# Performance work log

Hardware: AMD Instinct MI355X
Metric: run time of the kernel (lower is better)

The kernel has to match this reference:

```python
import jax, jax.numpy as jnp
import numpy as np

SR = 44100.0
J, Q = 12, 16
W0 = 2.0 * np.pi      # MorletWavelet.freq_to_w_at_s(1.0, s=1.0) -> w = 2*pi*f*s
N_SIG = 3.0           # wavelet support = +/- N_SIG standard deviations


def _make_wavelet_bank():
    """Morlet filter bank: J octaves, Q steps/octave, highest freq = nyquist.
    Returns centered, zero-padded real/imag filter stacks of shape (K, Lmax)."""
    dt = 1.0 / SR
    nyq = SR / 2.0
    wavelets = []
    for j in range(J):
        for q in range(Q):
            f = nyq / (2.0 ** (j + q / Q))
            s = 1.0 / f                      # center freq f = W0/(2*pi*s) = 1/s
            M = int(np.ceil(N_SIG * s * SR))  # half support in samples
            t = np.arange(-M, M + 1) * dt
            psi = (np.pi ** -0.25) / np.sqrt(s) \
                * np.exp(1j * W0 * t / s) * np.exp(-0.5 * (t / s) ** 2)
            psi = psi / np.sum(np.abs(psi))   # L1 normalization
            wavelets.append(psi.astype(np.complex64))
    Lmax = max(len(p) for p in wavelets)       # odd (2*M_max + 1)
    bank = np.zeros((len(wavelets), Lmax), np.complex64)
    for i, p in enumerate(wavelets):
        left = (Lmax - len(p)) // 2            # center-pad each wavelet
        bank[i, left:left + len(p)] = p
    return bank


def setup_inputs() -> dict:
    key = jax.random.key(0)
    x = jax.random.normal(key, (2, 1, 32768), dtype=jnp.float32)
    bank = _make_wavelet_bank()
    return {
        "x": x,
        "filt_real": jnp.asarray(bank.real, dtype=jnp.float32),
        "filt_imag": jnp.asarray(bank.imag, dtype=jnp.float32),
    }


def _scat1d(x, filt_real, filt_imag):
    # x: (B, 1, T); filters: (K, L) with L odd. Equivalent to the torch path:
    # pad input by L//2, cross-correlate (F.conv1d) with each complex wavelet,
    # take the modulus. Done via FFT (same math, efficient for ~47k-tap kernels).
    K, L = filt_real.shape
    B, C, T = x.shape  # C == 1 (squeeze_channels=True)
    P = L // 2
    xp = jnp.pad(x[:, 0, :], ((0, 0), (P, P)))       # (B, T + 2P)
    n_full = xp.shape[-1] + L - 1
    N = 1 << (n_full - 1).bit_length()               # next pow2 FFT size
    X = jnp.fft.rfft(xp, N)                          # (B, N//2+1)
    Gr = jnp.fft.rfft(filt_real[:, ::-1], N)         # flip -> corr via conv
    Gi = jnp.fft.rfft(filt_imag[:, ::-1], N)         # (K, N//2+1)
    lo = L - 1                                       # valid-corr offset
    yr = jnp.fft.irfft(X[:, None, :] * Gr[None], N)[..., lo:lo + T]
    yi = jnp.fft.irfft(X[:, None, :] * Gi[None], N)[..., lo:lo + T]
    return jnp.sqrt(yr * yr + yi * yi)               # (B, K, T) modulus


def reference(x, filt_real, filt_imag):
    return _scat1d(x, filt_real, filt_imag)
```

## Files before the change

### kernel.cpp

```cpp
#include <hip/hip_runtime.h>
#include <math.h>

#define T_LEN   32768
#define NK      192
#define NB      2
#define KDIR    48
#define MAXM    56
#define BBLK    9216
#define WBLK    3872
#define GRIDX   (BBLK + WBLK)

struct SParams {
  int m1e[144];
  int voff[144];
  int slot[144];
  int ab[9];
};

__device__ __forceinline__ int j2_of_q(int q) {
  return 4 + (q >= 5) + (q >= 10) + (q >= 15);
}

__global__ __launch_bounds__(256) void k_vtab(float* __restrict__ ws, SParams P) {
  int ki = blockIdx.y;
  int slotc = P.slot[ki];
  int M1e = P.m1e[ki];
  float* dst = ws + P.voff[ki];
  int nent = 2 * M1e + 2;
  int k = ki + 48;
  int j = k >> 4, q = k & 15;
  float sig = 2.f * exp2f((float)(16 * j + q) * 0.0625f);
  float s1 = sig * 0.86602540378f;
  float gc = -0.5f / (s1 * s1);
  float om = 6.28318530718f / sig;
  float norm = 1.f / (2.50662827463f * s1 * erff((float)M1e / (1.41421356237f * s1)));
  #pragma unroll
  for (int e0 = 0; e0 < 4; ++e0) {
    int e = blockIdx.x * 1024 + e0 * 256 + threadIdx.x;
    if (e >= slotc) continue;
    if (e >= nent) { dst[2 * e] = 0.f; dst[2 * e + 1] = 0.f; continue; }
    float mm = (float)(e - M1e);
    float g = __expf(gc * mm * mm) * norm;
    float sn, cs; __sincosf(om * mm, &sn, &cs);
    dst[2 * e] = g * cs;
    dst[2 * e + 1] = g * sn;
  }
}

__global__ __launch_bounds__(256) void k_s1(const float* __restrict__ x,
                                            float* __restrict__ ws, SParams P) {
  __shared__ float red[16];
  const float* xb0 = x;
  const float* xb1 = x + T_LEN;
  int bx = blockIdx.x;
  int tid = threadIdx.x;

  if (bx < BBLK) {
    int j, base;
    if (bx < 512)       { j = 11; base = 0; }
    else if (bx < 1280) { j = 10; base = 512; }
    else if (bx < 2560) { j = 9;  base = 1280; }
    else if (bx < 4864) { j = 8;  base = 2560; }
    else                { j = 7;  base = 4864; }
    int rem = bx - base;
    int q = rem & 15, nidx = rem >> 4;
    int ki = 16 * (j - 3) + q;
    int d = 1 << j, J2 = j2_of_q(q);
    int M1e = P.m1e[ki];
    const float* vt = ws + P.voff[ki];
    int nd = (nidx - J2) * d;
    int ustart = nd - M1e;
    int it0 = (-ustart) >> 9; if (it0 < 0) it0 = 0;
    int itend = ((T_LEN - 1 - ustart) >> 9) + 1;
    int niter = P.slot[ki] >> 9; if (niter > itend) niter = itend;
    float ar0 = 0.f, ai0 = 0.f, ar1 = 0.f, ai1 = 0.f;
    int it = it0;
    for (; it + 4 <= niter; it += 4) {
      int mt0 = 2 * tid + (it << 9);
      float4 v0 = *(const float4*)(vt + 2 * mt0);
      float4 v1 = *(const float4*)(vt + 2 * (mt0 + 512));
      float4 v2 = *(const float4*)(vt + 2 * (mt0 + 1024));
      float4 v3 = *(const float4*)(vt + 2 * (mt0 + 1536));
      int u0 = ustart + mt0, u1 = u0 + 512, u2 = u0 + 1024, u3 = u0 + 1536;
      int c0 = min(max(u0, 0), T_LEN - 2), c1 = min(max(u1, 0), T_LEN - 2);
      int c2 = min(max(u2, 0), T_LEN - 2), c3 = min(max(u3, 0), T_LEN - 2);
      float2 a0 = *(const float2*)(xb0 + c0);
      float2 a1 = *(const float2*)(xb0 + c1);
      float2 a2 = *(const float2*)(xb0 + c2);
      float2 a3 = *(const float2*)(xb0 + c3);
      float2 b0 = *(const float2*)(xb1 + c0);
      float2 b1 = *(const float2*)(xb1 + c1);
      float2 b2 = *(const float2*)(xb1 + c2);
      float2 b3 = *(const float2*)(xb1 + c3);
      bool k0 = (unsigned)u0 <= (unsigned)(T_LEN - 2);
      bool k1 = (unsigned)u1 <= (unsigned)(T_LEN - 2);
      bool k2 = (unsigned)u2 <= (unsigned)(T_LEN - 2);
      bool k3 = (unsigned)u3 <= (unsigned)(T_LEN - 2);
      float xa00 = k0 ? a0.x : 0.f, xa01 = k0 ? a0.y : 0.f;
      float xa10 = k1 ? a1.x : 0.f, xa11 = k1 ? a1.y : 0.f;
      float xa20 = k2 ? a2.x : 0.f, xa21 = k2 ? a2.y : 0.f;
      float xa30 = k3 ? a3.x : 0.f, xa31 = k3 ? a3.y : 0.f;
      float xb00 = k0 ? b0.x : 0.f, xb01 = k0 ? b0.y : 0.f;
      float xb10 = k1 ? b1.x : 0.f, xb11 = k1 ? b1.y : 0.f;
      float xb20 = k2 ? b2.x : 0.f, xb21 = k2 ? b2.y : 0.f;
      float xb30 = k3 ? b3.x : 0.f, xb31 = k3 ? b3.y : 0.f;
      ar0 += v0.x * xa00; ai0 += v0.y * xa00; ar0 += v0.z * xa01; ai0 += v0.w * xa01;
      ar1 += v0.x * xb00; ai1 += v0.y * xb00; ar1 += v0.z * xb01; ai1 += v0.w * xb01;
      ar0 += v1.x * xa10; ai0 += v1.y * xa10; ar0 += v1.z * xa11; ai0 += v1.w * xa11;
      ar1 += v1.x * xb10; ai1 += v1.y * xb10; ar1 += v1.z * xb11; ai1 += v1.w * xb11;
      ar0 += v2.x * xa20; ai0 += v2.y * xa20; ar0 += v2.z * xa21; ai0 += v2.w * xa21;
      ar1 += v2.x * xb20; ai1 += v2.y * xb20; ar1 += v2.z * xb21; ai1 += v2.w * xb21;
      ar0 += v3.x * xa30; ai0 += v3.y * xa30; ar0 += v3.z * xa31; ai0 += v3.w * xa31;
      ar1 += v3.x * xb30; ai1 += v3.y * xb30; ar1 += v3.z * xb31; ai1 += v3.w * xb31;
    }
    for (; it < niter; ++it) {
      int mt = 2 * tid + (it << 9);
      float4 v = *(const float4*)(vt + 2 * mt);
      int u = ustart + mt;
      int uc = min(max(u, 0), T_LEN - 2);
      float2 pa = *(const float2*)(xb0 + uc);
      float2 pb = *(const float2*)(xb1 + uc);
      bool ok = (unsigned)u <= (unsigned)(T_LEN - 2);
      float x0 = ok ? pa.x : 0.f, x1 = ok ? pa.y : 0.f;
      float y0 = ok ? pb.x : 0.f, y1 = ok ? pb.y : 0.f;
      ar0 += v.x * x0; ai0 += v.y * x0; ar0 += v.z * x1; ai0 += v.w * x1;
      ar1 += v.x * y0; ai1 += v.y * y0; ar1 += v.z * y1; ai1 += v.w * y1;
    }
#define RED4(s_) ar0 += __shfl_xor(ar0, s_, 64); ai0 += __shfl_xor(ai0, s_, 64); \
                 ar1 += __shfl_xor(ar1, s_, 64); ai1 += __shfl_xor(ai1, s_, 64);
    RED4(1) RED4(2) RED4(4) RED4(8) RED4(16) RED4(32)
#undef RED4
    int wv = tid >> 6;
    if ((tid & 63) == 0) {
      red[4 * wv] = ar0; red[4 * wv + 1] = ai0;
      red[4 * wv + 2] = ar1; red[4 * wv + 3] = ai1;
    }
    __syncthreads();
    if (tid == 0) {
      ar0 = red[0] + red[4] + red[8] + red[12];
      ai0 = red[1] + red[5] + red[9] + red[13];
      ar1 = red[2] + red[6] + red[10] + red[14];
      ai1 = red[3] + red[7] + red[11] + red[15];
      float rev = (float)nd * exp2f(-(float)(16 * (j + 1) + q) * 0.0625f);
      rev -= floorf(rev);
      float sn, cs; __sincosf(rev * 6.28318530718f, &sn, &cs);
      int Ncu = (32767 >> j) + 17;
      float* ap = ws + P.ab[j - 3] + (q * 2) * Ncu * 2;
      *(float2*)(ap + 2 * nidx) = make_float2(ar0 * cs - ai0 * sn, ar0 * sn + ai0 * cs);
      *(float2*)(ap + 2 * (Ncu + nidx)) = make_float2(ar1 * cs - ai1 * sn, ar1 * sn + ai1 * cs);
    }
  } else {
    int wv = tid >> 6, lane = tid & 63;
    int wid = (bx - BBLK) * 4 + wv;
    int j, base;
    if (wid < 1056)      { j = 6; base = 0; }
    else if (wid < 3136) { j = 5; base = 1056; }
    else if (wid < 7264) { j = 4; base = 3136; }
    else                 { j = 3; base = 7264; }
    int rem = wid - base;
    int q = rem & 15, tile = rem >> 4;
    int ki = 16 * (j - 3) + q;
    int d = 1 << j, J2 = j2_of_q(q);
    int M1e = P.m1e[ki];
    const float* vt = ws + P.voff[ki];
    int r = lane >> 3, p = lane & 7;
    int nidx = tile * 8 + r;
    int nd = (nidx - J2) * d;
    int ustart = nd - M1e;
    int it0 = (-ustart) >> 4; if (it0 < 0) it0 = 0;
    int itend = ((T_LEN - 1 - ustart) >> 4) + 1;
    int niter = P.slot[ki] >> 4; if (niter > itend) niter = itend;
    float ar0 = 0.f, ai0 = 0.f, ar1 = 0.f, ai1 = 0.f;
    int it = it0;
    int pb2 = 2 * p;
    for (; it + 4 <= niter; it += 4) {
      int mt0 = pb2 + (it << 4);
      float4 v0 = *(const float4*)(vt + 2 * mt0);
      float4 v1 = *(const float4*)(vt + 2 * (mt0 + 16));
      float4 v2 = *(const float4*)(vt + 2 * (mt0 + 32));
      float4 v3 = *(const float4*)(vt + 2 * (mt0 + 48));
      int u0 = ustart + mt0, u1 = u0 + 16, u2 = u0 + 32, u3 = u0 + 48;
      int c0 = min(max(u0, 0), T_LEN - 2), c1 = min(max(u1, 0), T_LEN - 2);
      int c2 = min(max(u2, 0), T_LEN - 2), c3 = min(max(u3, 0), T_LEN - 2);
      float2 a0 = *(const float2*)(xb0 + c0);
      float2 a1 = *(const float2*)(xb0 + c1);
      float2 a2 = *(const float2*)(xb0 + c2);
      float2 a3 = *(const float2*)(xb0 + c3);
      float2 b0 = *(const float2*)(xb1 + c0);
      float2 b1 = *(const float2*)(xb1 + c1);
      float2 b2 = *(const float2*)(xb1 + c2);
      float2 b3 = *(const float2*)(xb1 + c3);
      bool k0 = (unsigned)u0 <= (unsigned)(T_LEN - 2);
      bool k1 = (unsigned)u1 <= (unsigned)(T_LEN - 2);
      bool k2 = (unsigned)u2 <= (unsigned)(T_LEN - 2);
      bool k3 = (unsigned)u3 <= (unsigned)(T_LEN - 2);
      float xa00 = k0 ? a0.x : 0.f, xa01 = k0 ? a0.y : 0.f;
      float xa10 = k1 ? a1.x : 0.f, xa11 = k1 ? a1.y : 0.f;
      float xa20 = k2 ? a2.x : 0.f, xa21 = k2 ? a2.y : 0.f;
      float xa30 = k3 ? a3.x : 0.f, xa31 = k3 ? a3.y : 0.f;
      float xb00 = k0 ? b0.x : 0.f, xb01 = k0 ? b0.y : 0.f;
      float xb10 = k1 ? b1.x : 0.f, xb11 = k1 ? b1.y : 0.f;
      float xb20 = k2 ? b2.x : 0.f, xb21 = k2 ? b2.y : 0.f;
      float xb30 = k3 ? b3.x : 0.f, xb31 = k3 ? b3.y : 0.f;
      ar0 += v0.x * xa00; ai0 += v0.y * xa00; ar0 += v0.z * xa01; ai0 += v0.w * xa01;
      ar1 += v0.x * xb00; ai1 += v0.y * xb00; ar1 += v0.z * xb01; ai1 += v0.w * xb01;
      ar0 += v1.x * xa10; ai0 += v1.y * xa10; ar0 += v1.z * xa11; ai0 += v1.w * xa11;
      ar1 += v1.x * xb10; ai1 += v1.y * xb10; ar1 += v1.z * xb11; ai1 += v1.w * xb11;
      ar0 += v2.x * xa20; ai0 += v2.y * xa20; ar0 += v2.z * xa21; ai0 += v2.w * xa21;
      ar1 += v2.x * xb20; ai1 += v2.y * xb20; ar1 += v2.z * xb21; ai1 += v2.w * xb21;
      ar0 += v3.x * xa30; ai0 += v3.y * xa30; ar0 += v3.z * xa31; ai0 += v3.w * xa31;
      ar1 += v3.x * xb30; ai1 += v3.y * xb30; ar1 += v3.z * xb31; ai1 += v3.w * xb31;
    }
    for (; it < niter; ++it) {
      int mt = pb2 + (it << 4);
      float4 v = *(const float4*)(vt + 2 * mt);
      int u = ustart + mt;
      int uc = min(max(u, 0), T_LEN - 2);
      float2 pa = *(const float2*)(xb0 + uc);
      float2 pbv = *(const float2*)(xb1 + uc);
      bool ok = (unsigned)u <= (unsigned)(T_LEN - 2);
      float x0 = ok ? pa.x : 0.f, x1 = ok ? pa.y : 0.f;
      float y0 = ok ? pbv.x : 0.f, y1 = ok ? pbv.y : 0.f;
      ar0 += v.x * x0; ai0 += v.y * x0; ar0 += v.z * x1; ai0 += v.w * x1;
      ar1 += v.x * y0; ai1 += v.y * y0; ar1 += v.z * y1; ai1 += v.w * y1;
    }
#define RED4(s_) ar0 += __shfl_xor(ar0, s_, 64); ai0 += __shfl_xor(ai0, s_, 64); \
                 ar1 += __shfl_xor(ar1, s_, 64); ai1 += __shfl_xor(ai1, s_, 64);
    RED4(1) RED4(2) RED4(4)
#undef RED4
    if (p == 0) {
      float rev = (float)nd * exp2f(-(float)(16 * (j + 1) + q) * 0.0625f);
      rev -= floorf(rev);
      float sn, cs; __sincosf(rev * 6.28318530718f, &sn, &cs);
      int Ncu = (32767 >> j) + 17;
      float* ap = ws + P.ab[j - 3] + (q * 2) * Ncu * 2;
      *(float2*)(ap + 2 * nidx) = make_float2(ar0 * cs - ai0 * sn, ar0 * sn + ai0 * cs);
      *(float2*)(ap + 2 * (Ncu + nidx)) = make_float2(ar1 * cs - ai1 * sn, ar1 * sn + ai1 * cs);
    }
  }
}

__global__ __launch_bounds__(256) void k_stage2(const float* __restrict__ ws,
                                                float* __restrict__ out, SParams P) {
  int k = KDIR + blockIdx.y;
  int j = k >> 4, q = k & 15;
  int d = 1 << j;
  int J2 = j2_of_q(q);
  float sig = 2.f * exp2f((float)(16 * j + q) * 0.0625f);
  float s2 = sig * 0.5f;
  int Ncu = (32767 >> j) + 17;
  const float* A0 = ws + P.ab[j - 3] + (q * 2) * Ncu * 2;
  const float* A1 = A0 + Ncu * 2;
  int t0 = blockIdx.x * 256 + threadIdx.x;
  int phi = t0 & (d - 1);
  int nb0 = t0 >> j;
  int step = 8192 >> j;
  int ntap = 2 * J2 + 1;
  float fd = (float)d;
  float inv2 = 1.f / (s2 * s2);
  float u0 = (float)(phi + J2 * d);
  float eg = __expf(-0.5f * u0 * u0 * inv2);
  float mf = __expf((fd * u0 - 0.5f * fd * fd) * inv2);
  float qf = __expf(-fd * fd * inv2);
  float Z = 0.f;
  float sr0 = 0.f, si0 = 0.f, sr1 = 0.f, si1 = 0.f;
  float sr2 = 0.f, si2 = 0.f, sr3 = 0.f, si3 = 0.f;
  float tr0 = 0.f, ti0 = 0.f, tr1 = 0.f, ti1 = 0.f;
  float tr2 = 0.f, ti2 = 0.f, tr3 = 0.f, ti3 = 0.f;
  const float* Ap0 = A0 + 2 * nb0;
  const float* Ap1 = A1 + 2 * nb0;
  for (int rr = 0; rr < ntap; ++rr) {
    float w = eg; eg *= mf; mf *= qf; Z += w;
    float2 a0 = *(const float2*)(Ap0 + 2 * rr);
    float2 a1 = *(const float2*)(Ap0 + 2 * (rr + step));
    float2 a2 = *(const float2*)(Ap0 + 2 * (rr + 2 * step));
    float2 a3 = *(const float2*)(Ap0 + 2 * (rr + 3 * step));
    float2 b0 = *(const float2*)(Ap1 + 2 * rr);
    float2 b1 = *(const float2*)(Ap1 + 2 * (rr + step));
    float2 b2 = *(const float2*)(Ap1 + 2 * (rr + 2 * step));
    float2 b3 = *(const float2*)(Ap1 + 2 * (rr + 3 * step));
    sr0 += w * a0.x; si0 += w * a0.y; sr1 += w * a1.x; si1 += w * a1.y;
    sr2 += w * a2.x; si2 += w * a2.y; sr3 += w * a3.x; si3 += w * a3.y;
    tr0 += w * b0.x; ti0 += w * b0.y; tr1 += w * b1.x; ti1 += w * b1.y;
    tr2 += w * b2.x; ti2 += w * b2.y; tr3 += w * b3.x; ti3 += w * b3.y;
  }
  float zi = 1.f / Z;
  size_t ob0 = (size_t)k * T_LEN + t0;
  size_t ob1 = (size_t)(NK + k) * T_LEN + t0;
  out[ob0]         = sqrtf(sr0 * sr0 + si0 * si0) * zi;
  out[ob0 + 8192]  = sqrtf(sr1 * sr1 + si1 * si1) * zi;
  out[ob0 + 16384] = sqrtf(sr2 * sr2 + si2 * si2) * zi;
  out[ob0 + 24576] = sqrtf(sr3 * sr3 + si3 * si3) * zi;
  out[ob1]         = sqrtf(tr0 * tr0 + ti0 * ti0) * zi;
  out[ob1 + 8192]  = sqrtf(tr1 * tr1 + ti1 * ti1) * zi;
  out[ob1 + 16384] = sqrtf(tr2 * tr2 + ti2 * ti2) * zi;
  out[ob1 + 24576] = sqrtf(tr3 * tr3 + ti3 * ti3) * zi;
}

__global__ __launch_bounds__(256) void k_direct(const float* __restrict__ x,
                                               const float* __restrict__ fr,
                                               const float* __restrict__ fi,
                                               float* __restrict__ out, int Lmax) {
  int k = blockIdx.y;
  int b = blockIdx.z;
  int t0 = blockIdx.x * 1024;
  int j = k >> 4, q = k & 15;
  int M = (int)ceil(6.0 * exp2((double)j + (double)q * 0.0625)) + 2;
  int P = Lmax >> 1;
  __shared__ float xs[1024 + 2 * MAXM];
  __shared__ float frs[2 * MAXM + 1], fis[2 * MAXM + 1];
  int tid = threadIdx.x;
  int xlen = 1024 + 2 * M;
  const float* xb = x + b * T_LEN;
  for (int i = tid; i < xlen; i += 256) {
    int u = t0 - M + i;
    xs[i] = (u >= 0 && u < T_LEN) ? xb[u] : 0.f;
  }
  const float* frk = fr + (size_t)k * Lmax + (P - M);
  const float* fik = fi + (size_t)k * Lmax + (P - M);
  int tl = 2 * M + 1;
  for (int i = tid; i < tl; i += 256) { frs[i] = frk[i]; fis[i] = fik[i]; }
  __syncthreads();
  float ar[4] = {0.f, 0.f, 0.f, 0.f}, ai[4] = {0.f, 0.f, 0.f, 0.f};
  for (int tau = 0; tau < tl; ++tau) {
    float wr = frs[tau], wi = fis[tau];
    #pragma unroll
    for (int tt = 0; tt < 4; ++tt) {
      float xv = xs[tid + tt * 256 + tau];
      ar[tt] += wr * xv; ai[tt] += wi * xv;
    }
  }
  size_t ob = (size_t)(b * NK + k) * T_LEN + t0 + tid;
  #pragma unroll
  for (int tt = 0; tt < 4; ++tt)
    out[ob + tt * 256] = sqrtf(ar[tt] * ar[tt] + ai[tt] * ai[tt]);
}

extern "C" void kernel_launch(void* const* d_in, const int* in_sizes, int n_in,
                              void* d_out, int out_size, void* d_ws, size_t ws_size,
                              hipStream_t stream) {
  const float* x  = (const float*)d_in[0];
  const float* fr = (const float*)d_in[1];
  const float* fi = (const float*)d_in[2];
  float* out = (float*)d_out;
  float* ws  = (float*)d_ws;
  int Lmax = in_sizes[1] / NK;

  SParams Pm;
  int cur = 0, maxslot = 0;
  for (int ki = 0; ki < 144; ++ki) {
    int j = (ki + 48) >> 4, q = ki & 15;
    double sig = 2.0 * exp2(((double)(16 * j + q)) / 16.0);
    double s1 = sig * 0.86602540378443864676;
    int M1 = (int)ceil(3.5 * s1);
    int M1e = (M1 + 1) & ~1;
    int R = (j >= 7) ? 512 : 16;
    int slotc = (2 * M1e + 2 + R - 1) & ~(R - 1);
    Pm.m1e[ki] = M1e;
    Pm.voff[ki] = cur;
    Pm.slot[ki] = slotc;
    if (slotc > maxslot) maxslot = slotc;
    cur += 2 * slotc;
  }
  for (int j = 3; j <= 11; ++j) {
    Pm.ab[j - 3] = cur;
    cur += 32 * ((32767 >> j) + 17) * 2;
  }

  k_vtab<<<dim3((maxslot + 1023) / 1024, 144), dim3(256), 0, stream>>>(ws, Pm);
  k_s1<<<dim3(GRIDX), dim3(256), 0, stream>>>(x, ws, Pm);
  k_direct<<<dim3(T_LEN / 1024, KDIR, NB), dim3(256), 0, stream>>>(x, fr, fi, out, Lmax);
  k_stage2<<<dim3(T_LEN / (256 * 4), NK - KDIR), dim3(256), 0, stream>>>(ws, out, Pm);
}
```

Baseline: 253.5 us.

## Tile decimated convolution outputs per block with shared-memory input staging

Restructures the first-stage decimated convolution kernel so each block computes several output positions per scale, G for deep scales and 64 or 128 for shallow ones. The input window is staged once in shared memory (interleaved for both batches, padded to avoid bank conflicts) and the wavelet table is reused across outputs, replacing per-output global gathers and the reduction across the whole block. The direct short-filter kernel is also register-blocked to compute four consecutive outputs per thread with float4 loads and a vector store. This adds template-specialized code paths, more registers per thread (up to 64 accumulators), larger shared memory use, and a host-computed block partition table.

```diff
diff --git a/kernel.cpp b/kernel.cpp
--- a/kernel.cpp
+++ b/kernel.cpp
@@ -6,15 +6,13 @@
 #define NB      2
 #define KDIR    48
 #define MAXM    56
-#define BBLK    9216
-#define WBLK    3872
-#define GRIDX   (BBLK + WBLK)
 
 struct SParams {
   int m1e[144];
   int voff[144];
   int slot[144];
   int ab[9];
+  int jb[10];
 };
 
 __device__ __forceinline__ int j2_of_q(int q) {
@@ -47,196 +45,182 @@
   }
 }
 
-__global__ __launch_bounds__(256) void k_s1(const float* __restrict__ x,
-                                            float* __restrict__ ws, SParams P) {
-  __shared__ float red[16];
+
+template<int J, int G, int E>
+__device__ __forceinline__ void deep_path(const float* __restrict__ x,
+                                          float* __restrict__ ws, const SParams& P,
+                                          int q, int tile, int tid,
+                                          float* xs, float* red) {
+  constexpr int d = 1 << J;
+  constexpr int W = E + (G - 1) * d + 2;
+  const int ki = 16 * (J - 3) + q;
+  const int J2 = j2_of_q(q);
+  const int M1e = P.m1e[ki];
+  const int slot = P.slot[ki];
+  const float* vt = ws + P.voff[ki];
+  const int n0 = tile * G;
+  const int ubase0 = (n0 - J2) * d - M1e;
   const float* xb0 = x;
   const float* xb1 = x + T_LEN;
-  int bx = blockIdx.x;
-  int tid = threadIdx.x;
-
-  if (bx < BBLK) {
-    int j, base;
-    if (bx < 512)       { j = 11; base = 0; }
-    else if (bx < 1280) { j = 10; base = 512; }
-    else if (bx < 2560) { j = 9;  base = 1280; }
-    else if (bx < 4864) { j = 8;  base = 2560; }
-    else                { j = 7;  base = 4864; }
-    int rem = bx - base;
-    int q = rem & 15, nidx = rem >> 4;
-    int ki = 16 * (j - 3) + q;
-    int d = 1 << j, J2 = j2_of_q(q);
-    int M1e = P.m1e[ki];
-    const float* vt = ws + P.voff[ki];
-    int nd = (nidx - J2) * d;
-    int ustart = nd - M1e;
-    int it0 = (-ustart) >> 9; if (it0 < 0) it0 = 0;
-    int itend = ((T_LEN - 1 - ustart) >> 9) + 1;
-    int niter = P.slot[ki] >> 9; if (niter > itend) niter = itend;
-    float ar0 = 0.f, ai0 = 0.f, ar1 = 0.f, ai1 = 0.f;
-    int it = it0;
-    for (; it + 4 <= niter; it += 4) {
-      int mt0 = 2 * tid + (it << 9);
-      float4 v0 = *(const float4*)(vt + 2 * mt0);
-      float4 v1 = *(const float4*)(vt + 2 * (mt0 + 512));
-      float4 v2 = *(const float4*)(vt + 2 * (mt0 + 1024));
-      float4 v3 = *(const float4*)(vt + 2 * (mt0 + 1536));
-      int u0 = ustart + mt0, u1 = u0 + 512, u2 = u0 + 1024, u3 = u0 + 1536;
-      int c0 = min(max(u0, 0), T_LEN - 2), c1 = min(max(u1, 0), T_LEN - 2);
-      int c2 = min(max(u2, 0), T_LEN - 2), c3 = min(max(u3, 0), T_LEN - 2);
-      float2 a0 = *(const float2*)(xb0 + c0);
-      float2 a1 = *(const float2*)(xb0 + c1);
-      float2 a2 = *(const float2*)(xb0 + c2);
-      float2 a3 = *(const float2*)(xb0 + c3);
-      float2 b0 = *(const float2*)(xb1 + c0);
-      float2 b1 = *(const float2*)(xb1 + c1);
-      float2 b2 = *(const float2*)(xb1 + c2);
-      float2 b3 = *(const float2*)(xb1 + c3);
-      bool k0 = (unsigned)u0 <= (unsigned)(T_LEN - 2);
-      bool k1 = (unsigned)u1 <= (unsigned)(T_LEN - 2);
-      bool k2 = (unsigned)u2 <= (unsigned)(T_LEN - 2);
-      bool k3 = (unsigned)u3 <= (unsigned)(T_LEN - 2);
-      float xa00 = k0 ? a0.x : 0.f, xa01 = k0 ? a0.y : 0.f;
-      float xa10 = k1 ? a1.x : 0.f, xa11 = k1 ? a1.y : 0.f;
-      float xa20 = k2 ? a2.x : 0.f, xa21 = k2 ? a2.y : 0.f;
-      float xa30 = k3 ? a3.x : 0.f, xa31 = k3 ? a3.y : 0.f;
-      float xb00 = k0 ? b0.x : 0.f, xb01 = k0 ? b0.y : 0.f;
-      float xb10 = k1 ? b1.x : 0.f, xb11 = k1 ? b1.y : 0.f;
-      float xb20 = k2 ? b2.x : 0.f, xb21 = k2 ? b2.y : 0.f;
-      float xb30 = k3 ? b3.x : 0.f, xb31 = k3 ? b3.y : 0.f;
-      ar0 += v0.x * xa00; ai0 += v0.y * xa00; ar0 += v0.z * xa01; ai0 += v0.w * xa01;
-      ar1 += v0.x * xb00; ai1 += v0.y * xb00; ar1 += v0.z * xb01; ai1 += v0.w * xb01;
-      ar0 += v1.x * xa10; ai0 += v1.y * xa10; ar0 += v1.z * xa11; ai0 += v1.w * xa11;
-      ar1 += v1.x * xb10; ai1 += v1.y * xb10; ar1 += v1.z * xb11; ai1 += v1.w * xb11;
-      ar0 += v2.x * xa20; ai0 += v2.y * xa20; ar0 += v2.z * xa21; ai0 += v2.w * xa21;
-      ar1 += v2.x * xb20; ai1 += v2.y * xb20; ar1 += v2.z * xb21; ai1 += v2.w * xb21;
-      ar0 += v3.x * xa30; ai0 += v3.y * xa30; ar0 += v3.z * xa31; ai0 += v3.w * xa31;
-      ar1 += v3.x * xb30; ai1 += v3.y * xb30; ar1 += v3.z * xb31; ai1 += v3.w * xb31;
-    }
-    for (; it < niter; ++it) {
-      int mt = 2 * tid + (it << 9);
-      float4 v = *(const float4*)(vt + 2 * mt);
-      int u = ustart + mt;
-      int uc = min(max(u, 0), T_LEN - 2);
-      float2 pa = *(const float2*)(xb0 + uc);
-      float2 pb = *(const float2*)(xb1 + uc);
-      bool ok = (unsigned)u <= (unsigned)(T_LEN - 2);
-      float x0 = ok ? pa.x : 0.f, x1 = ok ? pa.y : 0.f;
-      float y0 = ok ? pb.x : 0.f, y1 = ok ? pb.y : 0.f;
-      ar0 += v.x * x0; ai0 += v.y * x0; ar0 += v.z * x1; ai0 += v.w * x1;
-      ar1 += v.x * y0; ai1 += v.y * y0; ar1 += v.z * y1; ai1 += v.w * y1;
-    }
-#define RED4(s_) ar0 += __shfl_xor(ar0, s_, 64); ai0 += __shfl_xor(ai0, s_, 64); \
-                 ar1 += __shfl_xor(ar1, s_, 64); ai1 += __shfl_xor(ai1, s_, 64);
-    RED4(1) RED4(2) RED4(4) RED4(8) RED4(16) RED4(32)
-#undef RED4
-    int wv = tid >> 6;
-    if ((tid & 63) == 0) {
-      red[4 * wv] = ar0; red[4 * wv + 1] = ai0;
-      red[4 * wv + 2] = ar1; red[4 * wv + 3] = ai1;
+
+  float acc[4 * G];
+  #pragma unroll
+  for (int i = 0; i < 4 * G; ++i) acc[i] = 0.f;
+
+  for (int e0 = 0; e0 < slot; e0 += E) {
+    int ub = ubase0 + e0;
+    if (ub >= T_LEN || ub + W <= 0) continue;
+    int Ech = slot - e0; if (Ech > E) Ech = E;
+    int Wn = Ech + (G - 1) * d + 2;
+    int Wh = (Wn + 1) >> 1;
+    for (int i = tid; i < Wh; i += 256) {
+      int u0 = ub + 2 * i;
+      bool ok = (unsigned)u0 <= (unsigned)(T_LEN - 2);
+      int uc = ok ? u0 : 0;
+      float2 a = *(const float2*)(xb0 + uc);
+      float2 b = *(const float2*)(xb1 + uc);
+      float4 w;
+      w.x = ok ? a.x : 0.f; w.y = ok ? b.x : 0.f;
+      w.z = ok ? a.y : 0.f; w.w = ok ? b.y : 0.f;
+      *(float4*)(xs + 4 * i) = w;
     }
     __syncthreads();
-    if (tid == 0) {
-      ar0 = red[0] + red[4] + red[8] + red[12];
-      ai0 = red[1] + red[5] + red[9] + red[13];
-      ar1 = red[2] + red[6] + red[10] + red[14];
-      ai1 = red[3] + red[7] + red[11] + red[15];
-      float rev = (float)nd * exp2f(-(float)(16 * (j + 1) + q) * 0.0625f);
+    int pend = Ech >> 9;
+    const float4* xp0 = (const float4*)xs + tid;
+    const float* vte = vt + 2 * e0 + 4 * tid;
+    for (int ps = 0; ps < pend; ++ps) {
+      float4 v = *(const float4*)(vte + (ps << 10));
+      const float4* xp = xp0 + (ps << 8);
+      #pragma unroll
+      for (int g = 0; g < G; ++g) {
+        float4 xv = xp[g * (d >> 1)];
+        acc[4 * g + 0] += v.x * xv.x + v.z * xv.z;
+        acc[4 * g + 1] += v.y * xv.x + v.w * xv.z;
+        acc[4 * g + 2] += v.x * xv.y + v.z * xv.w;
+        acc[4 * g + 3] += v.y * xv.y + v.w * xv.w;
+      }
+    }
+    __syncthreads();
+  }
+
+  #pragma unroll
+  for (int st = 1; st < 64; st <<= 1) {
+    #pragma unroll
+    for (int i = 0; i < 4 * G; ++i) acc[i] += __shfl_xor(acc[i], st, 64);
+  }
+  int wv = tid >> 6;
+  if ((tid & 63) == 0) {
+    #pragma unroll
+    for (int gg = 0; gg < G; ++gg)
+      *(float4*)(red + wv * 64 + 4 * gg) =
+        make_float4(acc[4 * gg], acc[4 * gg + 1], acc[4 * gg + 2], acc[4 * gg + 3]);
+  }
+  __syncthreads();
+  if (tid < 4 * G)
+    red[256 + tid] = red[tid] + red[64 + tid] + red[128 + tid] + red[192 + tid];
+  __syncthreads();
+  if (tid < G) {
+    int nidx = n0 + tid;
+    int Ncu = (32767 >> J) + 17;
+    if (nidx < Ncu) {
+      float ar0 = red[256 + 4 * tid], ai0 = red[256 + 4 * tid + 1];
+      float ar1 = red[256 + 4 * tid + 2], ai1 = red[256 + 4 * tid + 3];
+      float ndf = (float)((nidx - J2) * d);
+      float rev = ndf * exp2f(-(float)(16 * (J + 1) + q) * 0.0625f);
       rev -= floorf(rev);
       float sn, cs; __sincosf(rev * 6.28318530718f, &sn, &cs);
-      int Ncu = (32767 >> j) + 17;
-      float* ap = ws + P.ab[j - 3] + (q * 2) * Ncu * 2;
+      float* ap = ws + P.ab[J - 3] + (q * 2) * Ncu * 2;
       *(float2*)(ap + 2 * nidx) = make_float2(ar0 * cs - ai0 * sn, ar0 * sn + ai0 * cs);
       *(float2*)(ap + 2 * (Ncu + nidx)) = make_float2(ar1 * cs - ai1 * sn, ar1 * sn + ai1 * cs);
     }
-  } else {
-    int wv = tid >> 6, lane = tid & 63;
-    int wid = (bx - BBLK) * 4 + wv;
-    int j, base;
-    if (wid < 1056)      { j = 6; base = 0; }
-    else if (wid < 3136) { j = 5; base = 1056; }
-    else if (wid < 7264) { j = 4; base = 3136; }
-    else                 { j = 3; base = 7264; }
-    int rem = wid - base;
-    int q = rem & 15, tile = rem >> 4;
-    int ki = 16 * (j - 3) + q;
-    int d = 1 << j, J2 = j2_of_q(q);
-    int M1e = P.m1e[ki];
-    const float* vt = ws + P.voff[ki];
-    int r = lane >> 3, p = lane & 7;
-    int nidx = tile * 8 + r;
-    int nd = (nidx - J2) * d;
-    int ustart = nd - M1e;
-    int it0 = (-ustart) >> 4; if (it0 < 0) it0 = 0;
-    int itend = ((T_LEN - 1 - ustart) >> 4) + 1;
-    int niter = P.slot[ki] >> 4; if (niter > itend) niter = itend;
-    float ar0 = 0.f, ai0 = 0.f, ar1 = 0.f, ai1 = 0.f;
-    int it = it0;
-    int pb2 = 2 * p;
-    for (; it + 4 <= niter; it += 4) {
-      int mt0 = pb2 + (it << 4);
-      float4 v0 = *(const float4*)(vt + 2 * mt0);
-      float4 v1 = *(const float4*)(vt + 2 * (mt0 + 16));
-      float4 v2 = *(const float4*)(vt + 2 * (mt0 + 32));
-      float4 v3 = *(const float4*)(vt + 2 * (mt0 + 48));
-      int u0 = ustart + mt0, u1 = u0 + 16, u2 = u0 + 32, u3 = u0 + 48;
-      int c0 = min(max(u0, 0), T_LEN - 2), c1 = min(max(u1, 0), T_LEN - 2);
-      int c2 = min(max(u2, 0), T_LEN - 2), c3 = min(max(u3, 0), T_LEN - 2);
-      float2 a0 = *(const float2*)(xb0 + c0);
-      float2 a1 = *(const float2*)(xb0 + c1);
-      float2 a2 = *(const float2*)(xb0 + c2);
-      float2 a3 = *(const float2*)(xb0 + c3);
-      float2 b0 = *(const float2*)(xb1 + c0);
-      float2 b1 = *(const float2*)(xb1 + c1);
-      float2 b2 = *(const float2*)(xb1 + c2);
-      float2 b3 = *(const float2*)(xb1 + c3);
-      bool k0 = (unsigned)u0 <= (unsigned)(T_LEN - 2);
-      bool k1 = (unsigned)u1 <= (unsigned)(T_LEN - 2);
-      bool k2 = (unsigned)u2 <= (unsigned)(T_LEN - 2);
-      bool k3 = (unsigned)u3 <= (unsigned)(T_LEN - 2);
-      float xa00 = k0 ? a0.x : 0.f, xa01 = k0 ? a0.y : 0.f;
-      float xa10 = k1 ? a1.x : 0.f, xa11 = k1 ? a1.y : 0.f;
-      float xa20 = k2 ? a2.x : 0.f, xa21 = k2 ? a2.y : 0.f;
-      float xa30 = k3 ? a3.x : 0.f, xa31 = k3 ? a3.y : 0.f;
-      float xb00 = k0 ? b0.x : 0.f, xb01 = k0 ? b0.y : 0.f;
-      float xb10 = k1 ? b1.x : 0.f, xb11 = k1 ? b1.y : 0.f;
-      float xb20 = k2 ? b2.x : 0.f, xb21 = k2 ? b2.y : 0.f;
-      float xb30 = k3 ? b3.x : 0.f, xb31 = k3 ? b3.y : 0.f;
-      ar0 += v0.x * xa00; ai0 += v0.y * xa00; ar0 += v0.z * xa01; ai0 += v0.w * xa01;
-      ar1 += v0.x * xb00; ai1 += v0.y * xb00; ar1 += v0.z * xb01; ai1 += v0.w * xb01;
-      ar0 += v1.x * xa10; ai0 += v1.y * xa10; ar0 += v1.z * xa11; ai0 += v1.w * xa11;
-      ar1 += v1.x * xb10; ai1 += v1.y * xb10; ar1 += v1.z * xb11; ai1 += v1.w * xb11;
-      ar0 += v2.x * xa20; ai0 += v2.y * xa20; ar0 += v2.z * xa21; ai0 += v2.w * xa21;
-      ar1 += v2.x * xb20; ai1 += v2.y * xb20; ar1 += v2.z * xb21; ai1 += v2.w * xb21;
-      ar0 += v3.x * xa30; ai0 += v3.y * xa30; ar0 += v3.z * xa31; ai0 += v3.w * xa31;
-      ar1 += v3.x * xb30; ai1 += v3.y * xb30; ar1 += v3.z * xb31; ai1 += v3.w * xb31;
-    }
-    for (; it < niter; ++it) {
-      int mt = pb2 + (it << 4);
-      float4 v = *(const float4*)(vt + 2 * mt);
-      int u = ustart + mt;
-      int uc = min(max(u, 0), T_LEN - 2);
-      float2 pa = *(const float2*)(xb0 + uc);
-      float2 pbv = *(const float2*)(xb1 + uc);
-      bool ok = (unsigned)u <= (unsigned)(T_LEN - 2);
-      float x0 = ok ? pa.x : 0.f, x1 = ok ? pa.y : 0.f;
-      float y0 = ok ? pbv.x : 0.f, y1 = ok ? pbv.y : 0.f;
-      ar0 += v.x * x0; ai0 += v.y * x0; ar0 += v.z * x1; ai0 += v.w * x1;
-      ar1 += v.x * y0; ai1 += v.y * y0; ar1 += v.z * y1; ai1 += v.w * y1;
-    }
-#define RED4(s_) ar0 += __shfl_xor(ar0, s_, 64); ai0 += __shfl_xor(ai0, s_, 64); \
-                 ar1 += __shfl_xor(ar1, s_, 64); ai1 += __shfl_xor(ai1, s_, 64);
-    RED4(1) RED4(2) RED4(4)
-#undef RED4
-    if (p == 0) {
-      float rev = (float)nd * exp2f(-(float)(16 * (j + 1) + q) * 0.0625f);
-      rev -= floorf(rev);
-      float sn, cs; __sincosf(rev * 6.28318530718f, &sn, &cs);
-      int Ncu = (32767 >> j) + 17;
-      float* ap = ws + P.ab[j - 3] + (q * 2) * Ncu * 2;
-      *(float2*)(ap + 2 * nidx) = make_float2(ar0 * cs - ai0 * sn, ar0 * sn + ai0 * cs);
-      *(float2*)(ap + 2 * (Ncu + nidx)) = make_float2(ar1 * cs - ai1 * sn, ar1 * sn + ai1 * cs);
-    }
+  }
+}
+
+template<int J, int TOUT>
+__device__ __forceinline__ void small_path(const float* __restrict__ x,
+                                           float* __restrict__ ws, const SParams& P,
+                                           int q, int tile, int tid,
+                                           float* xs, float* red) {
+  constexpr int d = 1 << J;
+  const int ki = 16 * (J - 3) + q;
+  const int J2 = j2_of_q(q);
+  const int M1e = P.m1e[ki];
+  const int nent = 2 * M1e + 2;
+  const float* vt = ws + P.voff[ki];
+  const int Ncu = (32767 >> J) + 17;
+  const int o0 = tile * TOUT;
+  const int ub = (o0 - J2) * d - M1e;
+  const int W = (TOUT - 1) * d + nent;
+  const int PS = W + (((W - 1) >> J) << 1) + 4;
+  const float* xb0 = x;
+  const float* xb1 = x + T_LEN;
+  for (int i = tid; i < W; i += 256) {
+    int u = ub + i;
+    bool ok = (unsigned)u < (unsigned)T_LEN;
+    int uc = ok ? u : 0;
+    float a = xb0[uc]; a = ok ? a : 0.f;
+    float bv = xb1[uc]; bv = ok ? bv : 0.f;
+    int ad = i + ((i >> J) << 1);
+    xs[ad] = a; xs[PS + ad] = bv;
+  }
+  __syncthreads();
+  int th = (TOUT == 128) ? tid : (tid & 127);
+  int o = th & (TOUT - 1);
+  int b = th / TOUT;
+  int half = (TOUT == 64) ? (tid >> 7) : 0;
+  int e_lo = 0, e_hi = nent;
+  if (TOUT == 64) {
+    int eh = (nent >> 2) << 1;
+    if (half) e_lo = eh; else e_hi = eh;
+  }
+  const float* pl = xs + b * PS;
+  int sb = o * d;
+  float ar = 0.f, ai = 0.f;
+  #pragma unroll 4
+  for (int e = e_lo; e < e_hi; e += 2) {
+    float4 v = *(const float4*)(vt + 2 * e);
+    int s = sb + e;
+    float2 xv = *(const float2*)(pl + s + ((s >> J) << 1));
+    ar += v.x * xv.x + v.z * xv.y;
+    ai += v.y * xv.x + v.w * xv.y;
+  }
+  if (TOUT == 64) {
+    if (tid >= 128) { red[2 * (tid - 128)] = ar; red[2 * (tid - 128) + 1] = ai; }
+    __syncthreads();
+    if (tid < 128) { ar += red[2 * tid]; ai += red[2 * tid + 1]; }
+  }
+  if (half == 0 && o0 + o < Ncu && (TOUT == 128 || tid < 128)) {
+    int nidx = o0 + o;
+    float ndf = (float)((nidx - J2) * d);
+    float rev = ndf * exp2f(-(float)(16 * (J + 1) + q) * 0.0625f);
+    rev -= floorf(rev);
+    float sn, cs; __sincosf(rev * 6.28318530718f, &sn, &cs);
+    float* ap = ws + P.ab[J - 3] + (q * 2) * Ncu * 2;
+    *(float2*)(ap + 2 * (b * Ncu + nidx)) = make_float2(ar * cs - ai * sn, ar * sn + ai * cs);
+  }
+}
+
+__global__ __launch_bounds__(256) void k_s1(const float* __restrict__ x,
+                                            float* __restrict__ ws, SParams P) {
+  __shared__ __align__(16) float xs[12292];
+  __shared__ __align__(16) float red[512];
+  int bx = blockIdx.x, tid = threadIdx.x;
+  int o = 0;
+  #pragma unroll
+  for (int t = 1; t < 9; ++t) if (bx >= P.jb[t]) o = t;
+  int j = 11 - o;
+  int rem = bx - P.jb[o];
+  int tile = rem >> 4, q = rem & 15;
+  switch (j) {
+    case 11: deep_path<11, 2, 4096>(x, ws, P, q, tile, tid, xs, red); break;
+    case 10: deep_path<10, 3, 3584>(x, ws, P, q, tile, tid, xs, red); break;
+    case 9:  deep_path<9, 4, 4096>(x, ws, P, q, tile, tid, xs, red); break;
+    case 8:  deep_path<8, 8, 4096>(x, ws, P, q, tile, tid, xs, red); break;
+    case 7:  deep_path<7, 16, 4096>(x, ws, P, q, tile, tid, xs, red); break;
+    case 6:  small_path<6, 64>(x, ws, P, q, tile, tid, xs, red); break;
+    case 5:  small_path<5, 128>(x, ws, P, q, tile, tid, xs, red); break;
+    case 4:  small_path<4, 128>(x, ws, P, q, tile, tid, xs, red); break;
+    default: small_path<3, 128>(x, ws, P, q, tile, tid, xs, red); break;
   }
 }
 
@@ -307,8 +291,8 @@
   int j = k >> 4, q = k & 15;
   int M = (int)ceil(6.0 * exp2((double)j + (double)q * 0.0625)) + 2;
   int P = Lmax >> 1;
-  __shared__ float xs[1024 + 2 * MAXM];
-  __shared__ float frs[2 * MAXM + 1], fis[2 * MAXM + 1];
+  __shared__ __align__(16) float xs[1024 + 2 * MAXM + 4];
+  __shared__ __align__(16) float frs[2 * MAXM + 4], fis[2 * MAXM + 4];
   int tid = threadIdx.x;
   int xlen = 1024 + 2 * M;
   const float* xb = x + b * T_LEN;
@@ -316,24 +300,39 @@
     int u = t0 - M + i;
     xs[i] = (u >= 0 && u < T_LEN) ? xb[u] : 0.f;
   }
+  if (tid < 4) xs[xlen + tid] = 0.f;
   const float* frk = fr + (size_t)k * Lmax + (P - M);
   const float* fik = fi + (size_t)k * Lmax + (P - M);
   int tl = 2 * M + 1;
   for (int i = tid; i < tl; i += 256) { frs[i] = frk[i]; fis[i] = fik[i]; }
+  if (tid < 3) { frs[tl + tid] = 0.f; fis[tl + tid] = 0.f; }
   __syncthreads();
-  float ar[4] = {0.f, 0.f, 0.f, 0.f}, ai[4] = {0.f, 0.f, 0.f, 0.f};
-  for (int tau = 0; tau < tl; ++tau) {
-    float wr = frs[tau], wi = fis[tau];
-    #pragma unroll
-    for (int tt = 0; tt < 4; ++tt) {
-      float xv = xs[tid + tt * 256 + tau];
-      ar[tt] += wr * xv; ai[tt] += wi * xv;
-    }
-  }
-  size_t ob = (size_t)(b * NK + k) * T_LEN + t0 + tid;
-  #pragma unroll
-  for (int tt = 0; tt < 4; ++tt)
-    out[ob + tt * 256] = sqrtf(ar[tt] * ar[tt] + ai[tt] * ai[tt]);
+  float ar0 = 0.f, ar1 = 0.f, ar2 = 0.f, ar3 = 0.f;
+  float ai0 = 0.f, ai1 = 0.f, ai2 = 0.f, ai3 = 0.f;
+  const float4* xsv = (const float4*)(xs + 4 * tid);
+  float4 w0 = xsv[0];
+  int groups = (tl + 3) >> 2;
+  for (int g = 0; g < groups; ++g) {
+    float4 w1 = xsv[g + 1];
+    float4 f4 = *(const float4*)(frs + 4 * g);
+    float4 h4 = *(const float4*)(fis + 4 * g);
+    ar0 += f4.x * w0.x + f4.y * w0.y + f4.z * w0.z + f4.w * w0.w;
+    ai0 += h4.x * w0.x + h4.y * w0.y + h4.z * w0.z + h4.w * w0.w;
+    ar1 += f4.x * w0.y + f4.y * w0.z + f4.z * w0.w + f4.w * w1.x;
+    ai1 += h4.x * w0.y + h4.y * w0.z + h4.z * w0.w + h4.w * w1.x;
+    ar2 += f4.x * w0.z + f4.y * w0.w + f4.z * w1.x + f4.w * w1.y;
+    ai2 += h4.x * w0.z + h4.y * w0.w + h4.z * w1.x + h4.w * w1.y;
+    ar3 += f4.x * w0.w + f4.y * w1.x + f4.z * w1.y + f4.w * w1.z;
+    ai3 += h4.x * w0.w + h4.y * w1.x + h4.z * w1.y + h4.w * w1.z;
+    w0 = w1;
+  }
+  size_t ob = (size_t)(b * NK + k) * T_LEN + t0 + 4 * tid;
+  float4 res;
+  res.x = sqrtf(ar0 * ar0 + ai0 * ai0);
+  res.y = sqrtf(ar1 * ar1 + ai1 * ai1);
+  res.z = sqrtf(ar2 * ar2 + ai2 * ai2);
+  res.w = sqrtf(ar3 * ar3 + ai3 * ai3);
+  *(float4*)(out + ob) = res;
 }
 
 extern "C" void kernel_launch(void* const* d_in, const int* in_sizes, int n_in,
@@ -354,8 +353,7 @@
     double s1 = sig * 0.86602540378443864676;
     int M1 = (int)ceil(3.5 * s1);
     int M1e = (M1 + 1) & ~1;
-    int R = (j >= 7) ? 512 : 16;
-    int slotc = (2 * M1e + 2 + R - 1) & ~(R - 1);
+    int slotc = (2 * M1e + 2 + 511) & ~511;
     Pm.m1e[ki] = M1e;
     Pm.voff[ki] = cur;
     Pm.slot[ki] = slotc;
@@ -366,9 +364,17 @@
     Pm.ab[j - 3] = cur;
     cur += 32 * ((32767 >> j) + 17) * 2;
   }
+  const int TO[9] = {2, 3, 4, 8, 16, 64, 128, 128, 128};
+  Pm.jb[0] = 0;
+  for (int o = 0; o < 9; ++o) {
+    int j = 11 - o;
+    int Ncu = (32767 >> j) + 17;
+    int tiles = (Ncu + TO[o] - 1) / TO[o];
+    Pm.jb[o + 1] = Pm.jb[o] + 16 * tiles;
+  }
 
   k_vtab<<<dim3((maxslot + 1023) / 1024, 144), dim3(256), 0, stream>>>(ws, Pm);
-  k_s1<<<dim3(GRIDX), dim3(256), 0, stream>>>(x, ws, Pm);
+  k_s1<<<dim3(Pm.jb[9]), dim3(256), 0, stream>>>(x, ws, Pm);
   k_direct<<<dim3(T_LEN / 1024, KDIR, NB), dim3(256), 0, stream>>>(x, fr, fi, out, Lmax);
   k_stage2<<<dim3(T_LEN / (256 * 4), NK - KDIR), dim3(256), 0, stream>>>(ws, out, Pm);
 }
```

Result: no change. 250.8 us (-1.1%).
